# Kernel tuning notes

Hardware: AMD Instinct MI355X
Metric: run time of the kernel (lower is better)

Reference implementation:

```python
import jax, jax.numpy as jnp
import numpy as np

N, E, D = 20000, 320000, 128


def _glorot(key, shape):
    fan_in, fan_out = shape[0], shape[-1]
    lim = jnp.sqrt(6.0 / (fan_in + fan_out)).astype(jnp.float32)
    return jax.random.uniform(key, shape, jnp.float32, -lim, lim)


def setup_inputs() -> dict:
    key = jax.random.key(0)
    ks = jax.random.split(key, 16)
    h = jax.random.normal(ks[0], (N, 1, D), jnp.float32)
    x = jax.random.normal(ks[1], (N, 3), jnp.float32)
    edge_index = jax.random.randint(ks[2], (2, E), 0, N, jnp.int64)
    # edge_mlp: SPDMLP(2D -> D -> D), 2 linear layers with ReLU between
    W1e = _glorot(ks[3], (2 * D, D)); b1e = jnp.zeros((D,), jnp.float32)
    W2e = _glorot(ks[4], (D, D));     b2e = jnp.zeros((D,), jnp.float32)
    # edge_inf: Linear(D, 1) + Sigmoid
    Wg = _glorot(ks[5], (D, 1));      bg = jnp.zeros((1,), jnp.float32)
    # node_mlp: SPDMLP(2D -> D -> D)
    W1n = _glorot(ks[6], (2 * D, D)); b1n = jnp.zeros((D,), jnp.float32)
    W2n = _glorot(ks[7], (D, D));     b2n = jnp.zeros((D,), jnp.float32)
    return {"h": h, "x": x, "edge_index": edge_index,
            "W1e": W1e, "b1e": b1e, "W2e": W2e, "b2e": b2e,
            "Wg": Wg, "bg": bg,
            "W1n": W1n, "b1n": b1n, "W2n": W2n, "b2n": b2n}


def _feature_joint(a, b):
    # a: [B, Na, Da], b: [B, Nb, Db] -> [B, Na+Nb, Da+Db] block-diagonal concat
    Da, Db = a.shape[2], b.shape[2]
    a_exp = jnp.concatenate([a, jnp.zeros(a.shape[:2] + (Db,), a.dtype)], axis=2)
    b_exp = jnp.concatenate([jnp.zeros(b.shape[:2] + (Da,), b.dtype), b], axis=2)
    return jnp.concatenate([a_exp, b_exp], axis=1)


def _mlp2(y, W1, b1, W2, b2):
    return jax.nn.relu(y @ W1 + b1) @ W2 + b2


def reference(h, x, edge_index, W1e, b1e, W2e, b2e, Wg, bg, W1n, b1n, W2n, b2n):
    src, dst = edge_index[0], edge_index[1]
    hi, hj = h[dst], h[src]                              # [E, 1, D] each
    mij = _mlp2(_feature_joint(hi, hj), W1e, b1e, W2e, b2e)  # [E, 2, D]
    eij = jax.nn.sigmoid(mij @ Wg + bg)                  # [E, 2, 1]
    mi = jax.ops.segment_sum(mij * eij, dst, num_segments=h.shape[0])  # [N, 2, D]
    h_new = h + _mlp2(_feature_joint(mi, h), W1n, b1n, W2n, b2n)       # [N, 3, D]
    return (h_new, x)
```

## Files before the change

### kernel.cpp

```cpp
#include <hip/hip_runtime.h>

#define D   128
#define SP  136
#define FS  132
#define NC  2
#define CAP 64

typedef __attribute__((ext_vector_type(8))) short bf16x8;
typedef __attribute__((ext_vector_type(4))) float f32x4;
typedef unsigned short u16;

__device__ __forceinline__ float sigmoidf(float v) { return 1.0f / (1.0f + __expf(-v)); }

__device__ __forceinline__ u16 f2bf(float x) {
    union { float f; unsigned u; } c; c.f = x;
    return (u16)((c.u + 0x7fffu + ((c.u >> 16) & 1u)) >> 16);
}
__device__ __forceinline__ float bflo(unsigned u) {
    union { unsigned v; float f; } c; c.v = u << 16; return c.f;
}
__device__ __forceinline__ float bfhi(unsigned u) {
    union { unsigned v; float f; } c; c.v = u & 0xffff0000u; return c.f;
}

__device__ __forceinline__ void layer_mfma(
    const u16* __restrict__ a_hi,
    const short* __restrict__ WbM, int lane, int ctbase, f32x4 acc[NC][2])
{
    #pragma unroll
    for (int ks = 0; ks < 4; ++ks) {
        bf16x8 ah[2];
        #pragma unroll
        for (int rt = 0; rt < 2; ++rt) {
            const int o = (rt * 16 + (lane & 15)) * SP + ks * 32 + (lane >> 4) * 8;
            ah[rt] = *reinterpret_cast<const bf16x8*>(a_hi + o);
        }
        #pragma unroll
        for (int c = 0; c < NC; ++c) {
            const bf16x8 bh = *reinterpret_cast<const bf16x8*>(
                WbM + ((ctbase + c) * 4 + ks) * 512 + lane * 8);
            #pragma unroll
            for (int rt = 0; rt < 2; ++rt)
                acc[c][rt] = __builtin_amdgcn_mfma_f32_16x16x32_bf16(ah[rt], bh, acc[c][rt], 0, 0, 0);
        }
    }
}

__device__ __forceinline__ void store_relu(
    const f32x4 acc[NC][2], const float b1v[NC],
    u16* __restrict__ t_hi, int lane, int ctbase)
{
    #pragma unroll
    for (int c = 0; c < NC; ++c)
        #pragma unroll
        for (int rt = 0; rt < 2; ++rt)
            #pragma unroll
            for (int rr = 0; rr < 4; ++rr) {
                const int row = rt * 16 + (lane >> 4) * 4 + rr;
                const int j   = (ctbase + c) * 16 + (lane & 15);
                t_hi[row * SP + j] = f2bf(fmaxf(acc[c][rt][rr] + b1v[c], 0.f));
            }
}

__device__ __forceinline__ void acc8(float* a, uint4 q) {
    a[0] += bflo(q.x); a[1] += bfhi(q.x);
    a[2] += bflo(q.y); a[3] += bfhi(q.y);
    a[4] += bflo(q.z); a[5] += bfhi(q.z);
    a[6] += bflo(q.w); a[7] += bfhi(q.w);
}

__device__ __forceinline__ void mlp_core(
    int base, int r, int N,
    const float* __restrict__ h,  const float* __restrict__ R0,
    const int* __restrict__ cnt,  const int* __restrict__ bucket,
    const u16* __restrict__ Q1b,  const short* __restrict__ Wb,
    const float* __restrict__ b1n, const float* __restrict__ b2n,
    float* __restrict__ out_h, u16* __restrict__ smem)
{
    u16* a_hi = smem;
    u16* t_hi = smem + 32 * SP;

    const int tid  = threadIdx.x, lane = tid & 63, w = tid >> 6;
    const int ctbase = w * NC;
    const int nl = tid >> 3, cg = tid & 7;

    if (r == 1) {
        int node = base + nl; if (node >= N) node = N - 1;
        int deg = cnt[node]; if (deg > CAP) deg = CAP;
        const int* __restrict__ bk = bucket + (size_t)node * CAP;
        const u16* __restrict__ Qc = Q1b + cg * 16;
        float a[16] = {0.f,0.f,0.f,0.f,0.f,0.f,0.f,0.f,0.f,0.f,0.f,0.f,0.f,0.f,0.f,0.f};
        for (int i = 0; i < deg; ++i) {
            const int s = bk[i];
            const uint4 qa = *reinterpret_cast<const uint4*>(Qc + (size_t)s * D);
            const uint4 qb = *reinterpret_cast<const uint4*>(Qc + (size_t)s * D + 8);
            acc8(a, qa); acc8(a + 8, qb);
        }
        union { u16 s[16]; uint4 v[2]; } ph;
        #pragma unroll
        for (int k = 0; k < 16; ++k) ph.s[k] = f2bf(a[k]);
        *reinterpret_cast<uint4*>(&a_hi[nl * SP + cg * 16])     = ph.v[0];
        *reinterpret_cast<uint4*>(&a_hi[nl * SP + cg * 16 + 8]) = ph.v[1];
    } else {
        const float* __restrict__ src = (r == 0) ? R0 : h;
        for (int idx = tid; idx < 32 * 32; idx += 256) {
            const int row = idx >> 5, c4 = (idx & 31) << 2;
            int node = base + row; if (node >= N) node = N - 1;
            float4 v = *reinterpret_cast<const float4*>(&src[(size_t)node * D + c4]);
            if (r == 0) {
                const float cv = (float)cnt[node];
                v.x *= cv; v.y *= cv; v.z *= cv; v.w *= cv;
            }
            ushort4 hi;
            hi.x = f2bf(v.x); hi.y = f2bf(v.y); hi.z = f2bf(v.z); hi.w = f2bf(v.w);
            *reinterpret_cast<ushort4*>(&a_hi[row * SP + c4]) = hi;
        }
    }
    __syncthreads();

    float b1v[NC], b2v[NC];
    #pragma unroll
    for (int c = 0; c < NC; ++c) {
        const int j = (ctbase + c) * 16 + (lane & 15);
        b1v[c] = b1n[j]; b2v[c] = b2n[j];
    }

    f32x4 acc[NC][2];
    #pragma unroll
    for (int c = 0; c < NC; ++c)
        #pragma unroll
        for (int rt = 0; rt < 2; ++rt) acc[c][rt] = (f32x4){0.f, 0.f, 0.f, 0.f};
    layer_mfma(a_hi, Wb + (size_t)((r == 2) ? 4 : 3) * 16384, lane, ctbase, acc);
    __syncthreads();
    store_relu(acc, b1v, t_hi, lane, ctbase);
    __syncthreads();

    f32x4 o[NC][2];
    #pragma unroll
    for (int c = 0; c < NC; ++c)
        #pragma unroll
        for (int rt = 0; rt < 2; ++rt) o[c][rt] = (f32x4){0.f, 0.f, 0.f, 0.f};
    layer_mfma(t_hi, Wb + (size_t)5 * 16384, lane, ctbase, o);
    __syncthreads();

    float* fs = reinterpret_cast<float*>(smem);
    #pragma unroll
    for (int c = 0; c < NC; ++c)
        #pragma unroll
        for (int rt = 0; rt < 2; ++rt)
            #pragma unroll
            for (int rr = 0; rr < 4; ++rr) {
                const int row = rt * 16 + (lane >> 4) * 4 + rr;
                const int j   = (ctbase + c) * 16 + (lane & 15);
                fs[row * FS + j] = o[c][rt][rr] + b2v[c];
            }
    __syncthreads();

    const int node = base + nl;
    if (node < N) {
        #pragma unroll
        for (int k = 0; k < 4; ++k) {
            float4 ov = *reinterpret_cast<const float4*>(&fs[nl * FS + cg * 16 + k * 4]);
            const float4 hv = *reinterpret_cast<const float4*>(&h[(size_t)node * D + cg * 16 + k * 4]);
            ov.x += hv.x; ov.y += hv.y; ov.z += hv.z; ov.w += hv.w;
            *reinterpret_cast<float4*>(&out_h[((size_t)node * 3 + r) * D + cg * 16 + k * 4]) = ov;
        }
    }
}

__global__ __launch_bounds__(256) void zero_repack_x_kernel(
    int* __restrict__ cnt, int N, int ZB,
    const float* __restrict__ W1e, const float* __restrict__ W2e,
    const float* __restrict__ W1n, const float* __restrict__ W2n,
    short* __restrict__ Wb,
    const float* __restrict__ x, float* __restrict__ out_x)
{
    const int RB = 48;
    if (blockIdx.x < (unsigned)ZB) {
        const int i = blockIdx.x * 256 + threadIdx.x;
        if (i < N) cnt[i] = 0;
        return;
    }
    if (blockIdx.x >= (unsigned)(ZB + RB)) {
        const int i4 = ((blockIdx.x - ZB - RB) * 256 + threadIdx.x) * 4;
        const int total = N * 3;
        if (i4 + 3 < total) {
            *reinterpret_cast<float4*>(&out_x[i4]) =
                *reinterpret_cast<const float4*>(&x[i4]);
        } else {
            for (int k = i4; k < total && k < i4 + 4; ++k) out_x[k] = x[k];
        }
        return;
    }
    const int gid = (blockIdx.x - ZB) * 256 + threadIdx.x;
    if (gid >= 6 * 8 * 4 * 64) return;
    const int lane = gid & 63;
    int t = gid >> 6;
    const int ks = t & 3; t >>= 2;
    const int ct = t & 7;
    const int m  = t >> 3;
    const float* src;
    switch (m) {
        case 0: src = W1e;             break;
        case 1: src = W1e + 128 * 128; break;
        case 2: src = W2e;             break;
        case 3: src = W1n;             break;
        case 4: src = W1n + 128 * 128; break;
        default: src = W2n;            break;
    }
    const int j  = ct * 16 + (lane & 15);
    const int k0 = ks * 32 + (lane >> 4) * 8;
    bf16x8 hi;
    #pragma unroll
    for (int e = 0; e < 8; ++e) hi[e] = (short)f2bf(src[(size_t)(k0 + e) * 128 + j]);
    *reinterpret_cast<bf16x8*>(Wb + (size_t)m * 16384 + (ct * 4 + ks) * 512 + lane * 8) = hi;
}

__global__ __launch_bounds__(256, 8) void pre_r2_scatter_kernel(
    const float* __restrict__ h, const short* __restrict__ Wb,
    const float* __restrict__ b1e, const float* __restrict__ b2e,
    const float* __restrict__ Wg,  const float* __restrict__ bg,
    const float* __restrict__ b1n, const float* __restrict__ b2n,
    float* __restrict__ R0, u16* __restrict__ Q1b, float* __restrict__ out_h,
    int N, int PB, int MB,
    const int* __restrict__ ei, int E, int* __restrict__ cnt, int* __restrict__ bucket)
{
    __shared__ __align__(16) u16 smem[2 * 32 * SP];
    __shared__ float red_s[4][32];

    const unsigned bid = blockIdx.x;

    if (bid >= (unsigned)(PB + MB)) {
        const int e = (bid - PB - MB) * 256 + threadIdx.x;
        if (e < E) {
            const int s = ei[e];
            const int d = ei[E + e];
            const int slot = atomicAdd(&cnt[d], 1);
            if (slot < CAP) bucket[(size_t)d * CAP + slot] = s;
        }
        return;
    }

    if (bid >= (unsigned)PB) {
        mlp_core((bid - PB) * 32, 2, N, h, R0, cnt, bucket, Q1b, Wb,
                 b1n, b2n, out_h, smem);
        return;
    }

    u16* a_hi = smem;
    u16* t_hi = smem + 32 * SP;
    const int tid  = threadIdx.x, lane = tid & 63, w = tid >> 6;
    const int hf   = bid & 1;
    const int base = (bid >> 1) * 32;
    const int ctbase = w * NC;

    for (int idx = tid; idx < 32 * 32; idx += 256) {
        const int row = idx >> 5, c4 = (idx & 31) << 2;
        int node = base + row; if (node >= N) node = N - 1;
        const float4 v = *reinterpret_cast<const float4*>(&h[(size_t)node * D + c4]);
        ushort4 hi;
        hi.x = f2bf(v.x); hi.y = f2bf(v.y); hi.z = f2bf(v.z); hi.w = f2bf(v.w);
        *reinterpret_cast<ushort4*>(&a_hi[row * SP + c4]) = hi;
    }
    __syncthreads();

    float b1v[NC], b2v[NC], wgv[NC];
    #pragma unroll
    for (int c = 0; c < NC; ++c) {
        const int j = (ctbase + c) * 16 + (lane & 15);
        b1v[c] = b1e[j]; b2v[c] = b2e[j]; wgv[c] = Wg[j];
    }
    const float bgv = bg[0];

    f32x4 acc[NC][2];
    #pragma unroll
    for (int c = 0; c < NC; ++c)
        #pragma unroll
        for (int rt = 0; rt < 2; ++rt) acc[c][rt] = (f32x4){0.f, 0.f, 0.f, 0.f};
    layer_mfma(a_hi, Wb + (size_t)hf * 16384, lane, ctbase, acc);
    __syncthreads();
    store_relu(acc, b1v, t_hi, lane, ctbase);
    __syncthreads();

    f32x4 p[NC][2];
    #pragma unroll
    for (int c = 0; c < NC; ++c)
        #pragma unroll
        for (int rt = 0; rt < 2; ++rt) p[c][rt] = (f32x4){0.f, 0.f, 0.f, 0.f};
    layer_mfma(t_hi, Wb + (size_t)2 * 16384, lane, ctbase, p);

    #pragma unroll
    for (int rt = 0; rt < 2; ++rt)
        #pragma unroll
        for (int rr = 0; rr < 4; ++rr) {
            float part = 0.f;
            #pragma unroll
            for (int c = 0; c < NC; ++c) part += (p[c][rt][rr] + b2v[c]) * wgv[c];
            #pragma unroll
            for (int m = 1; m <= 8; m <<= 1) part += __shfl_xor(part, m, 64);
            if ((lane & 15) == 0)
                red_s[w][rt * 16 + (lane >> 4) * 4 + rr] = part;
        }
    __syncthreads();

    float* fs = reinterpret_cast<float*>(smem);
    #pragma unroll
    for (int rt = 0; rt < 2; ++rt)
        #pragma unroll
        for (int rr = 0; rr < 4; ++rr) {
            const int row = rt * 16 + (lane >> 4) * 4 + rr;
            const float g = sigmoidf(red_s[0][row] + red_s[1][row] +
                                     red_s[2][row] + red_s[3][row] + bgv);
            #pragma unroll
            for (int c = 0; c < NC; ++c) {
                const int j = (ctbase + c) * 16 + (lane & 15);
                fs[row * FS + j] = (p[c][rt][rr] + b2v[c]) * g;
            }
        }
    __syncthreads();

    const int nl = tid >> 3, cg = tid & 7;
    const int node = base + nl;
    if (node < N) {
        if (hf == 0) {
            #pragma unroll
            for (int k = 0; k < 4; ++k) {
                const float4 v = *reinterpret_cast<const float4*>(&fs[nl * FS + cg * 16 + k * 4]);
                *reinterpret_cast<float4*>(&R0[(size_t)node * D + cg * 16 + k * 4]) = v;
            }
        } else {
            union { u16 s[16]; uint4 v[2]; } pk;
            #pragma unroll
            for (int k = 0; k < 16; ++k) pk.s[k] = f2bf(fs[nl * FS + cg * 16 + k]);
            *reinterpret_cast<uint4*>(&Q1b[(size_t)node * D + cg * 16])     = pk.v[0];
            *reinterpret_cast<uint4*>(&Q1b[(size_t)node * D + cg * 16 + 8]) = pk.v[1];
        }
    }
}

__global__ __launch_bounds__(256, 8) void mlp_r01_kernel(
    const float* __restrict__ h,  const float* __restrict__ R0,
    const int* __restrict__ cnt,  const int* __restrict__ bucket,
    const u16* __restrict__ Q1b,  const short* __restrict__ Wb,
    const float* __restrict__ b1n, const float* __restrict__ b2n,
    float* __restrict__ out_h, int N, int RT1)
{
    __shared__ __align__(16) u16 smem[2 * 32 * SP];

    int r, tile;
    if (blockIdx.x < (unsigned)RT1) { r = 1; tile = blockIdx.x; }
    else                            { r = 0; tile = blockIdx.x - RT1; }

    mlp_core(tile * 32, r, N, h, R0, cnt, bucket, Q1b, Wb,
             b1n, b2n, out_h, smem);
}

extern "C" void kernel_launch(void* const* d_in, const int* in_sizes, int n_in,
                              void* d_out, int out_size, void* d_ws, size_t ws_size,
                              hipStream_t stream)
{
    const float* h   = (const float*)d_in[0];
    const float* x   = (const float*)d_in[1];
    const int*   ei  = (const int*)d_in[2];
    const float* W1e = (const float*)d_in[3];
    const float* b1e = (const float*)d_in[4];
    const float* W2e = (const float*)d_in[5];
    const float* b2e = (const float*)d_in[6];
    const float* Wg  = (const float*)d_in[7];
    const float* bg  = (const float*)d_in[8];
    const float* W1n = (const float*)d_in[9];
    const float* b1n = (const float*)d_in[10];
    const float* W2n = (const float*)d_in[11];
    const float* b2n = (const float*)d_in[12];

    const int N = in_sizes[0] / D;
    const int E = in_sizes[2] / 2;

    float* R0     = (float*)d_ws;
    u16*   Q1b    = (u16*)(R0 + (size_t)N * D);
    short* Wb     = (short*)(Q1b + (size_t)N * D);
    int*   cnt    = (int*)(Wb + 6 * 16384);
    int*   bucket = cnt + N;

    float* out_h = (float*)d_out;
    float* out_x = out_h + (size_t)N * 3 * D;

    const int ntiles = (N + 31) / 32;
    const int ZB = (N + 255) / 256;
    const int RB = 48;
    const int XB = (N * 3 + 1023) / 1024;
    const int PB = ntiles * 2;
    const int MB = ntiles;
    const int SB = (E + 255) / 256;

    zero_repack_x_kernel<<<ZB + RB + XB, 256, 0, stream>>>(cnt, N, ZB,
                                                           W1e, W2e, W1n, W2n, Wb, x, out_x);
    pre_r2_scatter_kernel<<<PB + MB + SB, 256, 0, stream>>>(h, Wb, b1e, b2e, Wg, bg,
                                                            b1n, b2n, R0, Q1b, out_h,
                                                            N, PB, MB, ei, E, cnt, bucket);
    mlp_r01_kernel<<<ntiles * 2, 256, 0, stream>>>(h, R0, cnt, bucket, Q1b, Wb,
                                                   b1n, b2n, out_h, N, ntiles);
}
```

Baseline: 67.22 us.

## Fuse R0 edge-MLP path into node MLP kernel, drop R0 buffer

```diff
diff --git a/kernel.cpp b/kernel.cpp
--- a/kernel.cpp
+++ b/kernel.cpp
@@ -1,10 +1,10 @@
 #include <hip/hip_runtime.h>
 
-#define D   128
-#define SP  136
-#define FS  132
-#define NC  2
-#define CAP 64
+#define D    128
+#define SP   136
+#define FS   132
+#define NC   2
+#define CAP  64
 
 typedef __attribute__((ext_vector_type(8))) short bf16x8;
 typedef __attribute__((ext_vector_type(4))) float f32x4;
@@ -22,46 +22,6 @@
 __device__ __forceinline__ float bfhi(unsigned u) {
     union { unsigned v; float f; } c; c.v = u & 0xffff0000u; return c.f;
 }
-
-__device__ __forceinline__ void layer_mfma(
-    const u16* __restrict__ a_hi,
-    const short* __restrict__ WbM, int lane, int ctbase, f32x4 acc[NC][2])
-{
-    #pragma unroll
-    for (int ks = 0; ks < 4; ++ks) {
-        bf16x8 ah[2];
-        #pragma unroll
-        for (int rt = 0; rt < 2; ++rt) {
-            const int o = (rt * 16 + (lane & 15)) * SP + ks * 32 + (lane >> 4) * 8;
-            ah[rt] = *reinterpret_cast<const bf16x8*>(a_hi + o);
-        }
-        #pragma unroll
-        for (int c = 0; c < NC; ++c) {
-            const bf16x8 bh = *reinterpret_cast<const bf16x8*>(
-                WbM + ((ctbase + c) * 4 + ks) * 512 + lane * 8);
-            #pragma unroll
-            for (int rt = 0; rt < 2; ++rt)
-                acc[c][rt] = __builtin_amdgcn_mfma_f32_16x16x32_bf16(ah[rt], bh, acc[c][rt], 0, 0, 0);
-        }
-    }
-}
-
-__device__ __forceinline__ void store_relu(
-    const f32x4 acc[NC][2], const float b1v[NC],
-    u16* __restrict__ t_hi, int lane, int ctbase)
-{
-    #pragma unroll
-    for (int c = 0; c < NC; ++c)
-        #pragma unroll
-        for (int rt = 0; rt < 2; ++rt)
-            #pragma unroll
-            for (int rr = 0; rr < 4; ++rr) {
-                const int row = rt * 16 + (lane >> 4) * 4 + rr;
-                const int j   = (ctbase + c) * 16 + (lane & 15);
-                t_hi[row * SP + j] = f2bf(fmaxf(acc[c][rt][rr] + b1v[c], 0.f));
-            }
-}
-
 __device__ __forceinline__ void acc8(float* a, uint4 q) {
     a[0] += bflo(q.x); a[1] += bfhi(q.x);
     a[2] += bflo(q.y); a[3] += bfhi(q.y);
@@ -69,54 +29,66 @@
     a[6] += bflo(q.w); a[7] += bfhi(q.w);
 }
 
-__device__ __forceinline__ void mlp_core(
-    int base, int r, int N,
-    const float* __restrict__ h,  const float* __restrict__ R0,
-    const int* __restrict__ cnt,  const int* __restrict__ bucket,
-    const u16* __restrict__ Q1b,  const short* __restrict__ Wb,
+__device__ __forceinline__ void layer32(
+    const u16* __restrict__ plane, const short* __restrict__ WbM,
+    int lane, int ctbase, f32x4 acc[NC][2])
+{
+    #pragma unroll
+    for (int ks = 0; ks < 4; ++ks) {
+        bf16x8 a[2];
+        #pragma unroll
+        for (int rt = 0; rt < 2; ++rt)
+            a[rt] = *reinterpret_cast<const bf16x8*>(
+                plane + (rt * 16 + (lane & 15)) * SP + ks * 32 + (lane >> 4) * 8);
+        #pragma unroll
+        for (int c = 0; c < NC; ++c) {
+            const bf16x8 b = *reinterpret_cast<const bf16x8*>(
+                WbM + ((ctbase + c) * 4 + ks) * 512 + lane * 8);
+            #pragma unroll
+            for (int rt = 0; rt < 2; ++rt)
+                acc[c][rt] = __builtin_amdgcn_mfma_f32_16x16x32_bf16(a[rt], b, acc[c][rt], 0, 0, 0);
+        }
+    }
+}
+
+__device__ __forceinline__ void store_t32(
+    const f32x4 acc[NC][2], const float b1v[NC],
+    u16* __restrict__ dst, int lane, int ctbase)
+{
+    #pragma unroll
+    for (int c = 0; c < NC; ++c)
+        #pragma unroll
+        for (int rt = 0; rt < 2; ++rt)
+            #pragma unroll
+            for (int rr = 0; rr < 4; ++rr)
+                dst[(rt * 16 + (lane >> 4) * 4 + rr) * SP + (ctbase + c) * 16 + (lane & 15)] =
+                    f2bf(fmaxf(acc[c][rt][rr] + b1v[c], 0.f));
+}
+
+__device__ __forceinline__ void stage32(
+    const float* __restrict__ src, int base, int N, int tid, u16* __restrict__ plane)
+{
+    #pragma unroll
+    for (int it = 0; it < 4; ++it) {
+        const int idx = it * 256 + tid;
+        const int row = idx >> 5, c4 = (idx & 31) << 2;
+        int node = base + row; if (node >= N) node = N - 1;
+        const float4 v = *reinterpret_cast<const float4*>(&src[(size_t)node * D + c4]);
+        ushort4 s;
+        s.x = f2bf(v.x); s.y = f2bf(v.y); s.z = f2bf(v.z); s.w = f2bf(v.w);
+        *reinterpret_cast<ushort4*>(&plane[row * SP + c4]) = s;
+    }
+}
+
+__device__ __forceinline__ void mlp_tail(
+    const short* __restrict__ Wb, int mA,
     const float* __restrict__ b1n, const float* __restrict__ b2n,
-    float* __restrict__ out_h, u16* __restrict__ smem)
-{
-    u16* a_hi = smem;
-    u16* t_hi = smem + 32 * SP;
-
-    const int tid  = threadIdx.x, lane = tid & 63, w = tid >> 6;
+    const float* __restrict__ h, float* __restrict__ out_h,
+    int r, int base, int N,
+    u16* __restrict__ P1, u16* __restrict__ P2, u16* __restrict__ smem)
+{
+    const int tid = threadIdx.x, lane = tid & 63, w = tid >> 6;
     const int ctbase = w * NC;
-    const int nl = tid >> 3, cg = tid & 7;
-
-    if (r == 1) {
-        int node = base + nl; if (node >= N) node = N - 1;
-        int deg = cnt[node]; if (deg > CAP) deg = CAP;
-        const int* __restrict__ bk = bucket + (size_t)node * CAP;
-        const u16* __restrict__ Qc = Q1b + cg * 16;
-        float a[16] = {0.f,0.f,0.f,0.f,0.f,0.f,0.f,0.f,0.f,0.f,0.f,0.f,0.f,0.f,0.f,0.f};
-        for (int i = 0; i < deg; ++i) {
-            const int s = bk[i];
-            const uint4 qa = *reinterpret_cast<const uint4*>(Qc + (size_t)s * D);
-            const uint4 qb = *reinterpret_cast<const uint4*>(Qc + (size_t)s * D + 8);
-            acc8(a, qa); acc8(a + 8, qb);
-        }
-        union { u16 s[16]; uint4 v[2]; } ph;
-        #pragma unroll
-        for (int k = 0; k < 16; ++k) ph.s[k] = f2bf(a[k]);
-        *reinterpret_cast<uint4*>(&a_hi[nl * SP + cg * 16])     = ph.v[0];
-        *reinterpret_cast<uint4*>(&a_hi[nl * SP + cg * 16 + 8]) = ph.v[1];
-    } else {
-        const float* __restrict__ src = (r == 0) ? R0 : h;
-        for (int idx = tid; idx < 32 * 32; idx += 256) {
-            const int row = idx >> 5, c4 = (idx & 31) << 2;
-            int node = base + row; if (node >= N) node = N - 1;
-            float4 v = *reinterpret_cast<const float4*>(&src[(size_t)node * D + c4]);
-            if (r == 0) {
-                const float cv = (float)cnt[node];
-                v.x *= cv; v.y *= cv; v.z *= cv; v.w *= cv;
-            }
-            ushort4 hi;
-            hi.x = f2bf(v.x); hi.y = f2bf(v.y); hi.z = f2bf(v.z); hi.w = f2bf(v.w);
-            *reinterpret_cast<ushort4*>(&a_hi[row * SP + c4]) = hi;
-        }
-    }
-    __syncthreads();
 
     float b1v[NC], b2v[NC];
     #pragma unroll
@@ -130,9 +102,8 @@
     for (int c = 0; c < NC; ++c)
         #pragma unroll
         for (int rt = 0; rt < 2; ++rt) acc[c][rt] = (f32x4){0.f, 0.f, 0.f, 0.f};
-    layer_mfma(a_hi, Wb + (size_t)((r == 2) ? 4 : 3) * 16384, lane, ctbase, acc);
-    __syncthreads();
-    store_relu(acc, b1v, t_hi, lane, ctbase);
+    layer32(P1, Wb + (size_t)mA * 16384, lane, ctbase, acc);
+    store_t32(acc, b1v, P2, lane, ctbase);
     __syncthreads();
 
     f32x4 o[NC][2];
@@ -140,7 +111,7 @@
     for (int c = 0; c < NC; ++c)
         #pragma unroll
         for (int rt = 0; rt < 2; ++rt) o[c][rt] = (f32x4){0.f, 0.f, 0.f, 0.f};
-    layer_mfma(t_hi, Wb + (size_t)5 * 16384, lane, ctbase, o);
+    layer32(P2, Wb + (size_t)5 * 16384, lane, ctbase, o);
     __syncthreads();
 
     float* fs = reinterpret_cast<float*>(smem);
@@ -149,13 +120,12 @@
         #pragma unroll
         for (int rt = 0; rt < 2; ++rt)
             #pragma unroll
-            for (int rr = 0; rr < 4; ++rr) {
-                const int row = rt * 16 + (lane >> 4) * 4 + rr;
-                const int j   = (ctbase + c) * 16 + (lane & 15);
-                fs[row * FS + j] = o[c][rt][rr] + b2v[c];
-            }
-    __syncthreads();
-
+            for (int rr = 0; rr < 4; ++rr)
+                fs[(rt * 16 + (lane >> 4) * 4 + rr) * FS + (ctbase + c) * 16 + (lane & 15)] =
+                    o[c][rt][rr] + b2v[c];
+    __syncthreads();
+
+    const int nl = tid >> 3, cg = tid & 7;
     const int node = base + nl;
     if (node < N) {
         #pragma unroll
@@ -216,22 +186,25 @@
     *reinterpret_cast<bf16x8*>(Wb + (size_t)m * 16384 + (ct * 4 + ks) * 512 + lane * 8) = hi;
 }
 
-__global__ __launch_bounds__(256, 8) void pre_r2_scatter_kernel(
+__global__ __launch_bounds__(256, 4) void k2_pre_r2_scatter(
     const float* __restrict__ h, const short* __restrict__ Wb,
     const float* __restrict__ b1e, const float* __restrict__ b2e,
     const float* __restrict__ Wg,  const float* __restrict__ bg,
     const float* __restrict__ b1n, const float* __restrict__ b2n,
-    float* __restrict__ R0, u16* __restrict__ Q1b, float* __restrict__ out_h,
-    int N, int PB, int MB,
+    u16* __restrict__ Q1b, float* __restrict__ out_h,
+    int N, int QB, int MB,
     const int* __restrict__ ei, int E, int* __restrict__ cnt, int* __restrict__ bucket)
 {
     __shared__ __align__(16) u16 smem[2 * 32 * SP];
     __shared__ float red_s[4][32];
+    u16* P1 = smem;
+    u16* P2 = smem + 32 * SP;
 
     const unsigned bid = blockIdx.x;
-
-    if (bid >= (unsigned)(PB + MB)) {
-        const int e = (bid - PB - MB) * 256 + threadIdx.x;
+    const int tid = threadIdx.x, lane = tid & 63, w = tid >> 6;
+
+    if (bid >= (unsigned)(QB + MB)) {
+        const int e = (bid - QB - MB) * 256 + tid;
         if (e < E) {
             const int s = ei[e];
             const int d = ei[E + e];
@@ -241,27 +214,17 @@
         return;
     }
 
-    if (bid >= (unsigned)PB) {
-        mlp_core((bid - PB) * 32, 2, N, h, R0, cnt, bucket, Q1b, Wb,
-                 b1n, b2n, out_h, smem);
+    if (bid >= (unsigned)QB) {
+        const int base = (bid - QB) * 32;
+        stage32(h, base, N, tid, P1);
+        __syncthreads();
+        mlp_tail(Wb, 4, b1n, b2n, h, out_h, 2, base, N, P1, P2, smem);
         return;
     }
 
-    u16* a_hi = smem;
-    u16* t_hi = smem + 32 * SP;
-    const int tid  = threadIdx.x, lane = tid & 63, w = tid >> 6;
-    const int hf   = bid & 1;
-    const int base = (bid >> 1) * 32;
+    const int base = bid * 32;
     const int ctbase = w * NC;
-
-    for (int idx = tid; idx < 32 * 32; idx += 256) {
-        const int row = idx >> 5, c4 = (idx & 31) << 2;
-        int node = base + row; if (node >= N) node = N - 1;
-        const float4 v = *reinterpret_cast<const float4*>(&h[(size_t)node * D + c4]);
-        ushort4 hi;
-        hi.x = f2bf(v.x); hi.y = f2bf(v.y); hi.z = f2bf(v.z); hi.w = f2bf(v.w);
-        *reinterpret_cast<ushort4*>(&a_hi[row * SP + c4]) = hi;
-    }
+    stage32(h, base, N, tid, P1);
     __syncthreads();
 
     float b1v[NC], b2v[NC], wgv[NC];
@@ -277,9 +240,8 @@
     for (int c = 0; c < NC; ++c)
         #pragma unroll
         for (int rt = 0; rt < 2; ++rt) acc[c][rt] = (f32x4){0.f, 0.f, 0.f, 0.f};
-    layer_mfma(a_hi, Wb + (size_t)hf * 16384, lane, ctbase, acc);
-    __syncthreads();
-    store_relu(acc, b1v, t_hi, lane, ctbase);
+    layer32(P1, Wb + (size_t)1 * 16384, lane, ctbase, acc);
+    store_t32(acc, b1v, P2, lane, ctbase);
     __syncthreads();
 
     f32x4 p[NC][2];
@@ -287,7 +249,7 @@
     for (int c = 0; c < NC; ++c)
         #pragma unroll
         for (int rt = 0; rt < 2; ++rt) p[c][rt] = (f32x4){0.f, 0.f, 0.f, 0.f};
-    layer_mfma(t_hi, Wb + (size_t)2 * 16384, lane, ctbase, p);
+    layer32(P2, Wb + (size_t)2 * 16384, lane, ctbase, p);
 
     #pragma unroll
     for (int rt = 0; rt < 2; ++rt)
@@ -303,7 +265,6 @@
         }
     __syncthreads();
 
-    float* fs = reinterpret_cast<float*>(smem);
     #pragma unroll
     for (int rt = 0; rt < 2; ++rt)
         #pragma unroll
@@ -312,47 +273,133 @@
             const float g = sigmoidf(red_s[0][row] + red_s[1][row] +
                                      red_s[2][row] + red_s[3][row] + bgv);
             #pragma unroll
-            for (int c = 0; c < NC; ++c) {
-                const int j = (ctbase + c) * 16 + (lane & 15);
-                fs[row * FS + j] = (p[c][rt][rr] + b2v[c]) * g;
-            }
+            for (int c = 0; c < NC; ++c)
+                P1[row * SP + (ctbase + c) * 16 + (lane & 15)] =
+                    f2bf((p[c][rt][rr] + b2v[c]) * g);
         }
     __syncthreads();
 
     const int nl = tid >> 3, cg = tid & 7;
     const int node = base + nl;
     if (node < N) {
-        if (hf == 0) {
-            #pragma unroll
-            for (int k = 0; k < 4; ++k) {
-                const float4 v = *reinterpret_cast<const float4*>(&fs[nl * FS + cg * 16 + k * 4]);
-                *reinterpret_cast<float4*>(&R0[(size_t)node * D + cg * 16 + k * 4]) = v;
-            }
-        } else {
-            union { u16 s[16]; uint4 v[2]; } pk;
-            #pragma unroll
-            for (int k = 0; k < 16; ++k) pk.s[k] = f2bf(fs[nl * FS + cg * 16 + k]);
-            *reinterpret_cast<uint4*>(&Q1b[(size_t)node * D + cg * 16])     = pk.v[0];
-            *reinterpret_cast<uint4*>(&Q1b[(size_t)node * D + cg * 16 + 8]) = pk.v[1];
-        }
-    }
-}
-
-__global__ __launch_bounds__(256, 8) void mlp_r01_kernel(
-    const float* __restrict__ h,  const float* __restrict__ R0,
+        const uint4 v0 = *reinterpret_cast<const uint4*>(&P1[nl * SP + cg * 16]);
+        const uint4 v1 = *reinterpret_cast<const uint4*>(&P1[nl * SP + cg * 16 + 8]);
+        *reinterpret_cast<uint4*>(&Q1b[(size_t)node * D + cg * 16])     = v0;
+        *reinterpret_cast<uint4*>(&Q1b[(size_t)node * D + cg * 16 + 8]) = v1;
+    }
+}
+
+__global__ __launch_bounds__(256, 4) void k3_r1_r0(
+    const float* __restrict__ h,  const u16* __restrict__ Q1b,
+    const short* __restrict__ Wb,
+    const float* __restrict__ b1e, const float* __restrict__ b2e,
+    const float* __restrict__ Wg,  const float* __restrict__ bg,
+    const float* __restrict__ b1n, const float* __restrict__ b2n,
     const int* __restrict__ cnt,  const int* __restrict__ bucket,
-    const u16* __restrict__ Q1b,  const short* __restrict__ Wb,
-    const float* __restrict__ b1n, const float* __restrict__ b2n,
-    float* __restrict__ out_h, int N, int RT1)
+    float* __restrict__ out_h, int N, int RT)
 {
     __shared__ __align__(16) u16 smem[2 * 32 * SP];
-
-    int r, tile;
-    if (blockIdx.x < (unsigned)RT1) { r = 1; tile = blockIdx.x; }
-    else                            { r = 0; tile = blockIdx.x - RT1; }
-
-    mlp_core(tile * 32, r, N, h, R0, cnt, bucket, Q1b, Wb,
-             b1n, b2n, out_h, smem);
+    __shared__ float red_s[4][32];
+    u16* P1 = smem;
+    u16* P2 = smem + 32 * SP;
+
+    const int tid = threadIdx.x, lane = tid & 63, w = tid >> 6;
+    const int ctbase = w * NC;
+
+    if (blockIdx.x < (unsigned)RT) {
+        const int base = blockIdx.x * 32;
+        const int nl = tid >> 3, cg = tid & 7;
+        int node = base + nl; if (node >= N) node = N - 1;
+        int deg = cnt[node]; if (deg > CAP) deg = CAP;
+        const int* __restrict__ bk = bucket + (size_t)node * CAP;
+        const u16* __restrict__ Qc = Q1b + cg * 16;
+        float a[16] = {0.f,0.f,0.f,0.f,0.f,0.f,0.f,0.f,0.f,0.f,0.f,0.f,0.f,0.f,0.f,0.f};
+        int i = 0;
+        for (; i + 1 < deg; i += 2) {
+            const int s0 = bk[i], s1 = bk[i + 1];
+            const uint4 qa0 = *reinterpret_cast<const uint4*>(Qc + (size_t)s0 * D);
+            const uint4 qb0 = *reinterpret_cast<const uint4*>(Qc + (size_t)s0 * D + 8);
+            const uint4 qa1 = *reinterpret_cast<const uint4*>(Qc + (size_t)s1 * D);
+            const uint4 qb1 = *reinterpret_cast<const uint4*>(Qc + (size_t)s1 * D + 8);
+            acc8(a, qa0); acc8(a + 8, qb0);
+            acc8(a, qa1); acc8(a + 8, qb1);
+        }
+        if (i < deg) {
+            const int s = bk[i];
+            const uint4 qa = *reinterpret_cast<const uint4*>(Qc + (size_t)s * D);
+            const uint4 qb = *reinterpret_cast<const uint4*>(Qc + (size_t)s * D + 8);
+            acc8(a, qa); acc8(a + 8, qb);
+        }
+        #pragma unroll
+        for (int k4 = 0; k4 < 4; ++k4) {
+            ushort4 s4;
+            s4.x = f2bf(a[k4 * 4 + 0]); s4.y = f2bf(a[k4 * 4 + 1]);
+            s4.z = f2bf(a[k4 * 4 + 2]); s4.w = f2bf(a[k4 * 4 + 3]);
+            *reinterpret_cast<ushort4*>(&P1[nl * SP + cg * 16 + k4 * 4]) = s4;
+        }
+        __syncthreads();
+        mlp_tail(Wb, 3, b1n, b2n, h, out_h, 1, base, N, P1, P2, smem);
+        return;
+    }
+
+    const int base = (blockIdx.x - RT) * 32;
+    stage32(h, base, N, tid, P1);
+    __syncthreads();
+
+    float b1v[NC], b2v[NC], wgv[NC];
+    #pragma unroll
+    for (int c = 0; c < NC; ++c) {
+        const int j = (ctbase + c) * 16 + (lane & 15);
+        b1v[c] = b1e[j]; b2v[c] = b2e[j]; wgv[c] = Wg[j];
+    }
+    const float bgv = bg[0];
+
+    f32x4 acc[NC][2];
+    #pragma unroll
+    for (int c = 0; c < NC; ++c)
+        #pragma unroll
+        for (int rt = 0; rt < 2; ++rt) acc[c][rt] = (f32x4){0.f, 0.f, 0.f, 0.f};
+    layer32(P1, Wb, lane, ctbase, acc);
+    store_t32(acc, b1v, P2, lane, ctbase);
+    __syncthreads();
+
+    f32x4 p[NC][2];
+    #pragma unroll
+    for (int c = 0; c < NC; ++c)
+        #pragma unroll
+        for (int rt = 0; rt < 2; ++rt) p[c][rt] = (f32x4){0.f, 0.f, 0.f, 0.f};
+    layer32(P2, Wb + (size_t)2 * 16384, lane, ctbase, p);
+
+    #pragma unroll
+    for (int rt = 0; rt < 2; ++rt)
+        #pragma unroll
+        for (int rr = 0; rr < 4; ++rr) {
+            float part = 0.f;
+            #pragma unroll
+            for (int c = 0; c < NC; ++c) part += (p[c][rt][rr] + b2v[c]) * wgv[c];
+            #pragma unroll
+            for (int m = 1; m <= 8; m <<= 1) part += __shfl_xor(part, m, 64);
+            if ((lane & 15) == 0)
+                red_s[w][rt * 16 + (lane >> 4) * 4 + rr] = part;
+        }
+    __syncthreads();
+
+    #pragma unroll
+    for (int rt = 0; rt < 2; ++rt)
+        #pragma unroll
+        for (int rr = 0; rr < 4; ++rr) {
+            const int row = rt * 16 + (lane >> 4) * 4 + rr;
+            const float g = sigmoidf(red_s[0][row] + red_s[1][row] +
+                                     red_s[2][row] + red_s[3][row] + bgv);
+            int node2 = base + row; if (node2 >= N) node2 = N - 1;
+            const float cv = (float)cnt[node2];
+            #pragma unroll
+            for (int c = 0; c < NC; ++c)
+                P1[row * SP + (ctbase + c) * 16 + (lane & 15)] =
+                    f2bf(cv * (p[c][rt][rr] + b2v[c]) * g);
+        }
+    __syncthreads();
+    mlp_tail(Wb, 3, b1n, b2n, h, out_h, 0, base, N, P1, P2, smem);
 }
 
 extern "C" void kernel_launch(void* const* d_in, const int* in_sizes, int n_in,
@@ -376,8 +423,7 @@
     const int N = in_sizes[0] / D;
     const int E = in_sizes[2] / 2;
 
-    float* R0     = (float*)d_ws;
-    u16*   Q1b    = (u16*)(R0 + (size_t)N * D);
+    u16*   Q1b    = (u16*)d_ws;
     short* Wb     = (short*)(Q1b + (size_t)N * D);
     int*   cnt    = (int*)(Wb + 6 * 16384);
     int*   bucket = cnt + N;
@@ -385,19 +431,19 @@
     float* out_h = (float*)d_out;
     float* out_x = out_h + (size_t)N * 3 * D;
 
-    const int ntiles = (N + 31) / 32;
+    const int nt = (N + 31) / 32;
     const int ZB = (N + 255) / 256;
     const int RB = 48;
     const int XB = (N * 3 + 1023) / 1024;
-    const int PB = ntiles * 2;
-    const int MB = ntiles;
+    const int QB = nt;
+    const int MB = nt;
     const int SB = (E + 255) / 256;
 
     zero_repack_x_kernel<<<ZB + RB + XB, 256, 0, stream>>>(cnt, N, ZB,
                                                            W1e, W2e, W1n, W2n, Wb, x, out_x);
-    pre_r2_scatter_kernel<<<PB + MB + SB, 256, 0, stream>>>(h, Wb, b1e, b2e, Wg, bg,
-                                                            b1n, b2n, R0, Q1b, out_h,
-                                                            N, PB, MB, ei, E, cnt, bucket);
-    mlp_r01_kernel<<<ntiles * 2, 256, 0, stream>>>(h, R0, cnt, bucket, Q1b, Wb,
-                                                   b1n, b2n, out_h, N, ntiles);
-}
+    k2_pre_r2_scatter<<<QB + MB + SB, 256, 0, stream>>>(h, Wb, b1e, b2e, Wg, bg,
+                                                        b1n, b2n, Q1b, out_h,
+                                                        N, QB, MB, ei, E, cnt, bucket);
+    k3_r1_r0<<<nt * 2, 256, 0, stream>>>(h, Q1b, Wb, b1e, b2e, Wg, bg,
+                                         b1n, b2n, cnt, bucket, out_h, N, nt);
+}
```

After: 56.31 us, median of 3. 1.19x faster.
